# Kernel tuning notes

Measured on AMD Instinct MI355X. Metric: run time of the kernel, lower is better.

## Reference

```python
import jax, jax.numpy as jnp
import numpy as np

INPUT_SIZE, HIDDEN, OUTPUT, NUM_LAYERS = 128, 512, 64, 2
BATCH, SEQ = 64, 256


def setup_inputs() -> dict:
    key = jax.random.key(0)
    ks = jax.random.split(key, 4 * NUM_LAYERS + 3)
    s = 1.0 / np.sqrt(HIDDEN)  # PyTorch LSTM/Linear init scale
    inp = {"x": jax.random.normal(ks[0], (BATCH, SEQ, INPUT_SIZE), dtype=jnp.float32)}
    in_sz = INPUT_SIZE
    for l in range(NUM_LAYERS):
        k0, k1, k2, k3 = ks[1 + 4 * l:5 + 4 * l]
        inp[f"W_ih_{l}"] = jax.random.uniform(k0, (4 * HIDDEN, in_sz), minval=-s, maxval=s, dtype=jnp.float32)
        inp[f"W_hh_{l}"] = jax.random.uniform(k1, (4 * HIDDEN, HIDDEN), minval=-s, maxval=s, dtype=jnp.float32)
        inp[f"b_ih_{l}"] = jax.random.uniform(k2, (4 * HIDDEN,), minval=-s, maxval=s, dtype=jnp.float32)
        inp[f"b_hh_{l}"] = jax.random.uniform(k3, (4 * HIDDEN,), minval=-s, maxval=s, dtype=jnp.float32)
        in_sz = HIDDEN
    inp["W_fc"] = jax.random.uniform(ks[-2], (OUTPUT, HIDDEN), minval=-s, maxval=s, dtype=jnp.float32)
    inp["b_fc"] = jax.random.uniform(ks[-1], (OUTPUT,), minval=-s, maxval=s, dtype=jnp.float32)
    return inp


def _lstm_layer(x, W_ih, W_hh, b_ih, b_hh):
    # x: [B, T, D]. Precompute input-side gates for all timesteps (one big GEMM).
    B = x.shape[0]
    H = W_hh.shape[1]
    xg = jnp.einsum('btd,gd->btg', x, W_ih) + b_ih + b_hh  # [B, T, 4H]
    xg = jnp.swapaxes(xg, 0, 1)  # [T, B, 4H]

    def step(carry, xt):
        h, c = carry
        g = xt + h @ W_hh.T  # [B, 4H]; gate order i, f, g, o (PyTorch)
        i = jax.nn.sigmoid(g[:, 0 * H:1 * H])
        f = jax.nn.sigmoid(g[:, 1 * H:2 * H])
        gg = jnp.tanh(g[:, 2 * H:3 * H])
        o = jax.nn.sigmoid(g[:, 3 * H:4 * H])
        c = f * c + i * gg
        h = o * jnp.tanh(c)
        return (h, c), h

    h0 = jnp.zeros((B, H), dtype=x.dtype)
    (_, _), hs = jax.lax.scan(step, (h0, h0), xg)
    return jnp.swapaxes(hs, 0, 1)  # [B, T, H]


def reference(x, W_ih_0, W_hh_0, b_ih_0, b_hh_0, W_ih_1, W_hh_1, b_ih_1, b_hh_1, W_fc, b_fc):
    h = _lstm_layer(x, W_ih_0, W_hh_0, b_ih_0, b_hh_0)
    h = _lstm_layer(h, W_ih_1, W_hh_1, b_ih_1, b_hh_1)
    last = h[:, -1, :]  # [B, H]
    return last @ W_fc.T + b_fc  # [B, OUTPUT]
```

## Files before the change

### kernel.cpp

```cpp
#include <hip/hip_runtime.h>


#define NB    64
#define SEQL  256
#define INF   128
#define HID   512
#define OUTN  64
#define NWG   256
#define NT    256
#define NCNT  32
#define CADD  (NWG / NCNT)
#define PBOUND 8192

typedef __attribute__((ext_vector_type(8))) short  short8;
typedef __attribute__((ext_vector_type(4))) float  floatx4;
typedef unsigned short u16;
typedef unsigned long long u64;

#define TIE4(N, x0,x1,x2,x3)                                                \
  asm volatile("s_waitcnt vmcnt(" N ")" : "+v"(x0), "+v"(x1), "+v"(x2), "+v"(x3))
#define TIE3(N, x0,x1,x2)                                                   \
  asm volatile("s_waitcnt vmcnt(" N ")" : "+v"(x0), "+v"(x1), "+v"(x2))
#define TIE2(N, x0,x1)                                                      \
  asm volatile("s_waitcnt vmcnt(" N ")" : "+v"(x0), "+v"(x1))

#define MFMA(ACC, A, B) \
  ACC = __builtin_amdgcn_mfma_f32_16x16x32_bf16((A), (B), ACC, 0, 0, 0)

__device__ __forceinline__ u16 f2bf(float f) {
  union { float f; unsigned u; } v; v.f = f;
  return (u16)((v.u + 0x7FFFu + ((v.u >> 16) & 1u)) >> 16);
}
__device__ __forceinline__ float bf2f(u16 s) {
  union { unsigned u; float f; } v; v.u = ((unsigned)s) << 16;
  return v.f;
}
__device__ __forceinline__ float sigf(float v) {
  return __builtin_amdgcn_rcpf(1.f + __expf(-v));
}
__device__ __forceinline__ float tanh_fast(float v) {
  float cv = fminf(fmaxf(v, -15.f), 15.f);
  float e = __expf(2.f * cv);
  return (e - 1.f) * __builtin_amdgcn_rcpf(e + 1.f);
}

__device__ __forceinline__ short8 ldh(const u16* p) {
  short8 d;
  asm volatile("global_load_dwordx4 %0, %1, off sc0 sc1" : "=v"(d) : "v"(p));
  return d;
}
__device__ __forceinline__ void st8c(u16* p, u64 v) {
  __hip_atomic_store((u64*)p, v, __ATOMIC_RELAXED, __HIP_MEMORY_SCOPE_AGENT);
}

__device__ __forceinline__ int swz(int gi) {
  return (gi * 16) ^ (((gi >> 6) & 7) << 4);
}

__device__ __forceinline__ void wait_ge(const unsigned* f0, int thr0,
                                        const unsigned* f1, int thr1) {
  const int lane = threadIdx.x & 63;
  const unsigned* fp = nullptr;
  int thr = 0;
  if (lane < 16)      { fp = f0 + lane;        thr = thr0; }
  else if (lane < 32) { fp = f1 + (lane - 16); thr = thr1; }
  if (thr <= 0) fp = nullptr;
  for (int i = 0; i < PBOUND; ++i) {
    int v = 0x7fffffff;
    if (fp) v = (int)__hip_atomic_load(fp, __ATOMIC_RELAXED,
                                       __HIP_MEMORY_SCOPE_AGENT);
    if (__all(v >= thr)) break;
    if (i > 2048) __builtin_amdgcn_s_sleep(2);
  }
  __builtin_amdgcn_sched_barrier(0);
  asm volatile("" ::: "memory");
}

__device__ __forceinline__ void grid_bar_once(unsigned* leaf, int w) {
  asm volatile("s_waitcnt vmcnt(0)" ::: "memory");
  __syncthreads();
  if (threadIdx.x == 0)
    __hip_atomic_fetch_add(&leaf[(w & (NCNT - 1)) * 32], 1u, __ATOMIC_RELAXED,
                           __HIP_MEMORY_SCOPE_AGENT);
  if (threadIdx.x < 64) {
    const int lane = threadIdx.x & 63;
    for (int i = 0; i < (1 << 16); ++i) {
      unsigned v = CADD;
      if (lane < NCNT)
        v = __hip_atomic_load(&leaf[lane * 32], __ATOMIC_RELAXED,
                              __HIP_MEMORY_SCOPE_AGENT);
      if (__all(v >= CADD)) break;
      __builtin_amdgcn_s_sleep(1);
    }
  }
  __syncthreads();
}

__device__ __forceinline__ floatx4 xpose4(floatx4 v, int jb0, int jb1) {
  floatx4 t;
#pragma unroll
  for (int r = 0; r < 4; ++r) t[r] = __shfl_xor(v[r], 1);
  floatx4 u;
  u[0] = jb0 ? t[1] : v[0];
  u[1] = jb0 ? v[1] : t[0];
  u[2] = jb0 ? t[3] : v[2];
  u[3] = jb0 ? v[3] : t[2];
  floatx4 s;
#pragma unroll
  for (int r = 0; r < 4; ++r) s[r] = __shfl_xor(u[r], 2);
  floatx4 w_;
  w_[0] = jb1 ? s[2] : u[0];
  w_[1] = jb1 ? s[3] : u[1];
  w_[2] = jb1 ? u[2] : s[0];
  w_[3] = jb1 ? u[3] : s[1];
  return w_;
}

template <int KS, int KIN>
__device__ __forceinline__ void load_B(short8 (&Bf)[2][32],
                                       const float* __restrict__ Wih,
                                       const float* __restrict__ Whh,
                                       int li, int wv, int mrow, int quad) {
#pragma unroll
  for (int t2 = 0; t2 < 2; ++t2) {
    const int rowid = wv * 32 + t2 * 16 + mrow;
    const int r = (rowid & 3) * HID + 32 * li + (rowid >> 2);
    const float* wr = Wih + (size_t)r * KIN;
    const float* hr = Whh + (size_t)r * HID - KIN;
#pragma unroll
    for (int ks = 0; ks < KS; ++ks) {
      short8 v;
#pragma unroll
      for (int j = 0; j < 8; ++j) {
        const int k = 32 * ks + quad * 8 + j;
        v[j] = (short)f2bf(k < KIN ? wr[k] : hr[k]);
      }
      Bf[t2][ks] = v;
    }
  }
}

__global__ __launch_bounds__(NT, 1) void lstm_groups(
    const float* __restrict__ x,
    const float* __restrict__ Wih0, const float* __restrict__ Whh0,
    const float* __restrict__ bih0, const float* __restrict__ bhh0,
    const float* __restrict__ Wih1, const float* __restrict__ Whh1,
    const float* __restrict__ bih1, const float* __restrict__ bhh1,
    const float* __restrict__ Wfc,  const float* __restrict__ bfc,
    float* __restrict__ out,
    unsigned* __restrict__ leaf,
    unsigned* __restrict__ flag0, unsigned* __restrict__ flag1,
    u16* __restrict__ h0r, u16* __restrict__ h1r, u16* __restrict__ xg)
{
  const int w = blockIdx.x, tid = threadIdx.x;
  const int lane = tid & 63, wv = tid >> 6;
  const int quad = lane >> 4, mrow = lane & 15;
  const int g = w & 7, m = w >> 3;
  const bool isL1 = (m >= 16);
  const int  li   = isL1 ? m - 16 : m;

  __shared__ u64   h_lds8[8][8];
  __shared__ float red[16][17];
  __shared__ short8 hA2[2][512];
  __shared__ short8 hB[512];
  char* hAc = (char*)hA2;
  char* hBc = (char*)hB;

#pragma unroll
  for (int i = 0; i < 8; ++i) {
    const int s = w * 8 + i, gs = s >> 8, ts = s & 255;
    u16* dst = xg + (size_t)(gs * 256 + ts) * 1024;
    const int b = tid >> 5, k0 = (tid & 31) * 4;
    const float* src = x + ((size_t)(8 * gs + b) * SEQL + ts) * INF + k0;
    union { u16 h[4]; u64 u; } pk;
#pragma unroll
    for (int j = 0; j < 4; ++j) pk.h[j] = f2bf(src[j]);
    st8c(dst + b * 128 + k0, pk.u);
  }

  short8 Bf[2][32];
  if (isL1) load_B<32, HID>(Bf, Wih1, Whh1, li, wv, mrow, quad);
  else      load_B<20, INF>(Bf, Wih0, Whh0, li, wv, mrow, quad);
  float bsA, bsB;
  {
    const int r0 = wv * 32 + mrow, r1 = r0 + 16;
    const int ra = (r0 & 3) * HID + 32 * li + (r0 >> 2);
    const int rb = (r1 & 3) * HID + 32 * li + (r1 >> 2);
    bsA = isL1 ? (bih1[ra] + bhh1[ra]) : (bih0[ra] + bhh0[ra]);
    bsB = isL1 ? (bih1[rb] + bhh1[rb]) : (bih0[rb] + bhh0[rb]);
  }

  grid_bar_once(leaf, w);

  unsigned* flag0g = flag0 + g * 64;
  unsigned* flag1g = flag1 + g * 64;
  u16* h0g = h0r + (size_t)g * 32768;
  u16* h1g = h1r + (size_t)g * 32768;
  const u16* xgg = xg + (size_t)g * 256 * 1024;

  const int q4 = quad;
  const int m4 = mrow >> 2, jg = mrow & 3;
  const int jb0 = jg & 1, jb1 = (jg >> 1) & 1;
  float cstA = 0.f, cstB = 0.f;
  const int ab = mrow & 7;
  const int koff = quad * 8;

  const bool ldr = (wv != 0);
  const int base = tid - 64;

  if (isL1) {
    wait_ge(flag0g, 1, flag1g, 0);
    short8 s0 = ldh(h0g + tid * 8);
    short8 s1 = ldh(h0g + (tid + 256) * 8);
    TIE2("0", s0, s1);
    *(short8*)(hAc + swz(tid)) = s0;
    *(short8*)(hAc + swz(tid + 256)) = s1;
    __syncthreads();
  }

  for (int t = 0; t < SEQL; ++t) {
    floatx4 a00 = {bsA, bsA, bsA, bsA}, a01 = {0,0,0,0};
    floatx4 a10 = {bsB, bsB, bsB, bsB}, a11 = {0,0,0,0};
    const int pb = (t & 1) * 8192;
    const int nb_ = ((t + 1) & 1) * 8192;

    if (!isL1) {
      const u16* xa = xgg + (size_t)t * 1024 + ab * 128 + koff;
      short8 x0 = *(const short8*)(xa +  0);
      short8 x1 = *(const short8*)(xa + 32);
      short8 x2 = *(const short8*)(xa + 64);
      short8 x3 = *(const short8*)(xa + 96);
      MFMA(a00,x0,Bf[0][0]);  MFMA(a10,x0,Bf[1][0]);
      MFMA(a01,x1,Bf[0][1]);  MFMA(a11,x1,Bf[1][1]);
      MFMA(a00,x2,Bf[0][2]);  MFMA(a10,x2,Bf[1][2]);
      MFMA(a01,x3,Bf[0][3]);  MFMA(a11,x3,Bf[1][3]);

      if (ldr) {
        wait_ge(flag0g, t, flag1g, t - 7);
        const u16* src = h0g + ((t + 7) & 7) * 4096;
        const bool g2 = (base < 128);
        short8 s0 = ldh(src + base * 8);
        short8 s1 = ldh(src + (base + 192) * 8);
        short8 s2;
        if (g2) s2 = ldh(src + (base + 384) * 8);
        if (g2) { TIE3("0", s0, s1, s2); }
        else    { TIE2("0", s0, s1); }
        *(short8*)(hAc + swz(base)) = s0;
        *(short8*)(hAc + swz(base + 192)) = s1;
        if (g2) *(short8*)(hAc + swz(base + 384)) = s2;
      }
      __syncthreads();

#pragma unroll
      for (int n = 0; n < 16; ++n) {
        const short8 fv = *(const short8*)(
            hAc + ((ab * 1024 + n * 64 + quad * 16) ^ (ab << 4)));
        if ((n & 1) == 0) { MFMA(a00, fv, Bf[0][4 + n]); MFMA(a10, fv, Bf[1][4 + n]); }
        else              { MFMA(a01, fv, Bf[0][4 + n]); MFMA(a11, fv, Bf[1][4 + n]); }
      }
    } else {
      short8 b0, b1, b2, p0, p1, p2;
      bool g2 = false;
      if (ldr) {
        const int thr0 = (t + 2 < 256) ? (t + 2) : 256;
        wait_ge(flag0g, thr0, flag1g, t);
        const u16* srcB = h1g + ((t + 7) & 7) * 4096;
        const u16* srcP = h0g + ((t + 1) & 7) * 4096;
        g2 = (base < 128);
        b0 = ldh(srcB + base * 8);
        b1 = ldh(srcB + (base + 192) * 8);
        if (g2) b2 = ldh(srcB + (base + 384) * 8);
        p0 = ldh(srcP + base * 8);
        p1 = ldh(srcP + (base + 192) * 8);
        if (g2) p2 = ldh(srcP + (base + 384) * 8);
      }

#pragma unroll
      for (int n = 0; n < 16; ++n) {
        const short8 fv = *(const short8*)(
            hAc + pb + ((ab * 1024 + n * 64 + quad * 16) ^ (ab << 4)));
        if ((n & 1) == 0) { MFMA(a00, fv, Bf[0][n]); MFMA(a10, fv, Bf[1][n]); }
        else              { MFMA(a01, fv, Bf[0][n]); MFMA(a11, fv, Bf[1][n]); }
      }

      if (ldr) {
        if (g2) { TIE3("3", b0, b1, b2); }
        else    { TIE2("2", b0, b1); }
        *(short8*)(hBc + swz(base)) = b0;
        *(short8*)(hBc + swz(base + 192)) = b1;
        if (g2) *(short8*)(hBc + swz(base + 384)) = b2;
        if (g2) { TIE3("0", p0, p1, p2); }
        else    { TIE2("0", p0, p1); }
        *(short8*)(hAc + nb_ + swz(base)) = p0;
        *(short8*)(hAc + nb_ + swz(base + 192)) = p1;
        if (g2) *(short8*)(hAc + nb_ + swz(base + 384)) = p2;
      }
      __syncthreads();

#pragma unroll
      for (int n = 0; n < 16; ++n) {
        const short8 fv = *(const short8*)(
            hBc + ((ab * 1024 + n * 64 + quad * 16) ^ (ab << 4)));
        if ((n & 1) == 0) { MFMA(a00, fv, Bf[0][16 + n]); MFMA(a10, fv, Bf[1][16 + n]); }
        else              { MFMA(a01, fv, Bf[0][16 + n]); MFMA(a11, fv, Bf[1][16 + n]); }
      }
    }

    const floatx4 vA = a00 + a01, vB = a10 + a11;
    if (lane < 32) {
      const floatx4 gA = xpose4(vA, jb0, jb1);
      const floatx4 gB = xpose4(vB, jb0, jb1);
      const float cA = sigf(gA[1]) * cstA + sigf(gA[0]) * tanh_fast(gA[2]);
      const float cB = sigf(gB[1]) * cstB + sigf(gB[0]) * tanh_fast(gB[2]);
      cstA = cA; cstB = cB;
      u16* hl = (u16*)&h_lds8[q4 * 4 + jg][0];
      hl[wv * 8 + m4]     = f2bf(sigf(gA[3]) * tanh_fast(cA));
      hl[wv * 8 + m4 + 4] = f2bf(sigf(gB[3]) * tanh_fast(cB));
    }
    __syncthreads();

    if (tid < 64) {
      const int b = tid >> 3, u8 = tid & 7;
      const u64 v = h_lds8[b][u8];
      u16* dst = (isL1 ? h1g : h0g) + (t & 7) * 4096 + b * 512 + li * 32 + u8 * 4;
      st8c(dst, v);
    }
    asm volatile("s_waitcnt vmcnt(0)" ::: "memory");
    if (tid == 0)
      __hip_atomic_store((isL1 ? flag1g : flag0g) + li, (unsigned)(t + 1),
                         __ATOMIC_RELAXED, __HIP_MEMORY_SCOPE_AGENT);
  }

  wait_ge(flag1g, 256, flag1g, 0);
  {
    const int bloc = m >> 2, oq = m & 3;
    const int ol = tid >> 4, ksub = tid & 15;
    const u16* hp = h1g + 7 * 4096 + bloc * 512 + ksub * 32;
    short8 v0 = ldh(hp),      v1 = ldh(hp + 8);
    short8 v2 = ldh(hp + 16), v3 = ldh(hp + 24);
    TIE4("0", v0, v1, v2, v3);
    const float* wr = Wfc + (size_t)(oq * 16 + ol) * HID + ksub * 32;
    float s = 0.f;
#pragma unroll
    for (int j = 0; j < 8; ++j) {
      s += bf2f((u16)v0[j]) * wr[j];
      s += bf2f((u16)v1[j]) * wr[8 + j];
      s += bf2f((u16)v2[j]) * wr[16 + j];
      s += bf2f((u16)v3[j]) * wr[24 + j];
    }
    red[ol][ksub] = s;
    __syncthreads();
    if (tid < 16) {
      float sum = 0.f;
#pragma unroll
      for (int j = 0; j < 16; ++j) sum += red[tid][j];
      out[(size_t)(8 * g + bloc) * OUTN + oq * 16 + tid] = sum + bfc[oq * 16 + tid];
    }
  }
}


extern "C" void kernel_launch(void* const* d_in, const int* in_sizes, int n_in,
                              void* d_out, int out_size, void* d_ws, size_t ws_size,
                              hipStream_t stream) {
  (void)in_sizes; (void)n_in; (void)out_size; (void)ws_size;

  char* ws = (char*)d_ws;
  unsigned* leaf  = (unsigned*)(ws + 256);
  unsigned* flag0 = (unsigned*)(ws + 8192);
  unsigned* flag1 = (unsigned*)(ws + 16384);
  u16* h0r = (u16*)(ws + 32768);
  u16* h1r = (u16*)(ws + 557056);
  u16* xg  = (u16*)(ws + 1081344);

  hipMemsetAsync(d_ws, 0, 1081344, stream);

  const float* x    = (const float*)d_in[0];
  const float* Wih0 = (const float*)d_in[1];
  const float* Whh0 = (const float*)d_in[2];
  const float* bih0 = (const float*)d_in[3];
  const float* bhh0 = (const float*)d_in[4];
  const float* Wih1 = (const float*)d_in[5];
  const float* Whh1 = (const float*)d_in[6];
  const float* bih1 = (const float*)d_in[7];
  const float* bhh1 = (const float*)d_in[8];
  const float* Wfc  = (const float*)d_in[9];
  const float* bfc  = (const float*)d_in[10];
  float* out = (float*)d_out;

  void* args[] = {
    (void*)&x,
    (void*)&Wih0, (void*)&Whh0, (void*)&bih0, (void*)&bhh0,
    (void*)&Wih1, (void*)&Whh1, (void*)&bih1, (void*)&bhh1,
    (void*)&Wfc,  (void*)&bfc,
    (void*)&out,
    (void*)&leaf, (void*)&flag0, (void*)&flag1,
    (void*)&h0r, (void*)&h1r, (void*)&xg
  };
  hipError_t err = hipLaunchCooperativeKernel((const void*)lstm_groups,
                                              dim3(NWG), dim3(NT), args, 0, stream);
  if (err != hipSuccess) {
    hipLaunchKernelGGL(lstm_groups, dim3(NWG), dim3(NT), 0, stream,
                       x, Wih0, Whh0, bih0, bhh0, Wih1, Whh1, bih1, bhh1,
                       Wfc, bfc, out, leaf, flag0, flag1, h0r, h1r, xg);
  }
}
```

Measured before the change: 948.8 us.

## Replace flag polling with sentinel-valid data polling on 16-slot hidden-state rings

Consumers stop waiting on per-step producer flags and instead poll the hidden-state ring data directly, treating 0xFFFF bf16 values as not-yet-written sentinels, so the flag round-trip is removed from the recurrent critical path. The rings grow from 8 to 16 slots with slot 0 as the zero initial state. Layer-1 work-groups re-poison consumed slots with the sentinel to allow reuse. This adds extra memsets, sentinel-reset traffic and tricky ordering that could race or break if a real hidden value ever encodes as 0xFFFF (a NaN pattern, so unlikely).

```diff
diff --git a/kernel.cpp b/kernel.cpp
--- a/kernel.cpp
+++ b/kernel.cpp
@@ -19,8 +19,6 @@
 
 #define TIE4(N, x0,x1,x2,x3)                                                \
   asm volatile("s_waitcnt vmcnt(" N ")" : "+v"(x0), "+v"(x1), "+v"(x2), "+v"(x3))
-#define TIE3(N, x0,x1,x2)                                                   \
-  asm volatile("s_waitcnt vmcnt(" N ")" : "+v"(x0), "+v"(x1), "+v"(x2))
 #define TIE2(N, x0,x1)                                                      \
   asm volatile("s_waitcnt vmcnt(" N ")" : "+v"(x0), "+v"(x1))
 
@@ -52,23 +50,25 @@
 __device__ __forceinline__ void st8c(u16* p, u64 v) {
   __hip_atomic_store((u64*)p, v, __ATOMIC_RELAXED, __HIP_MEMORY_SCOPE_AGENT);
 }
+__device__ __forceinline__ unsigned ldf(const unsigned* p) {
+  return __hip_atomic_load(p, __ATOMIC_RELAXED, __HIP_MEMORY_SCOPE_AGENT);
+}
+
+__device__ __forceinline__ bool valid8(short8 v) {
+  return ((u16)v[0] != 0xFFFFu) & ((u16)v[4] != 0xFFFFu);
+}
 
 __device__ __forceinline__ int swz(int gi) {
   return (gi * 16) ^ (((gi >> 6) & 7) << 4);
 }
 
-__device__ __forceinline__ void wait_ge(const unsigned* f0, int thr0,
-                                        const unsigned* f1, int thr1) {
+__device__ __forceinline__ void wait_ge(const unsigned* f, int thr) {
+  if (thr <= 0) return;
   const int lane = threadIdx.x & 63;
-  const unsigned* fp = nullptr;
-  int thr = 0;
-  if (lane < 16)      { fp = f0 + lane;        thr = thr0; }
-  else if (lane < 32) { fp = f1 + (lane - 16); thr = thr1; }
-  if (thr <= 0) fp = nullptr;
+  const unsigned* p = (lane < 16) ? f + lane : nullptr;
   for (int i = 0; i < PBOUND; ++i) {
     int v = 0x7fffffff;
-    if (fp) v = (int)__hip_atomic_load(fp, __ATOMIC_RELAXED,
-                                       __HIP_MEMORY_SCOPE_AGENT);
+    if (p) v = (int)ldf(p);
     if (__all(v >= thr)) break;
     if (i > 2048) __builtin_amdgcn_s_sleep(2);
   }
@@ -86,9 +86,7 @@
     const int lane = threadIdx.x & 63;
     for (int i = 0; i < (1 << 16); ++i) {
       unsigned v = CADD;
-      if (lane < NCNT)
-        v = __hip_atomic_load(&leaf[lane * 32], __ATOMIC_RELAXED,
-                              __HIP_MEMORY_SCOPE_AGENT);
+      if (lane < NCNT) v = ldf(&leaf[lane * 32]);
       if (__all(v >= CADD)) break;
       __builtin_amdgcn_s_sleep(1);
     }
@@ -194,8 +192,8 @@
 
   unsigned* flag0g = flag0 + g * 64;
   unsigned* flag1g = flag1 + g * 64;
-  u16* h0g = h0r + (size_t)g * 32768;
-  u16* h1g = h1r + (size_t)g * 32768;
+  u16* h0g = h0r + (size_t)g * 65536;
+  u16* h1g = h1r + (size_t)g * 65536;
   const u16* xgg = xg + (size_t)g * 256 * 1024;
 
   const int q4 = quad;
@@ -207,12 +205,20 @@
 
   const bool ldr = (wv != 0);
   const int base = tid - 64;
+  int c0 = -1, c1 = -1;
 
   if (isL1) {
-    wait_ge(flag0g, 1, flag1g, 0);
-    short8 s0 = ldh(h0g + tid * 8);
-    short8 s1 = ldh(h0g + (tid + 256) * 8);
-    TIE2("0", s0, s1);
+    const u16* sp = h0g + 1 * 4096;
+    short8 s0 = {}, s1 = {};
+    bool done = false;
+    for (int it = 0; it < PBOUND && !done; ++it) {
+      s0 = ldh(sp + tid * 8);
+      s1 = ldh(sp + (tid + 256) * 8);
+      TIE2("0", s0, s1);
+      done = __all(valid8(s0) & valid8(s1));
+      if (it > 2048) __builtin_amdgcn_s_sleep(2);
+    }
+    __builtin_amdgcn_sched_barrier(0);
     *(short8*)(hAc + swz(tid)) = s0;
     *(short8*)(hAc + swz(tid + 256)) = s1;
     __syncthreads();
@@ -223,6 +229,7 @@
     floatx4 a10 = {bsB, bsB, bsB, bsB}, a11 = {0,0,0,0};
     const int pb = (t & 1) * 8192;
     const int nb_ = ((t + 1) & 1) * 8192;
+    const int thr = t - 8;
 
     if (!isL1) {
       const u16* xa = xgg + (size_t)t * 1024 + ab * 128 + koff;
@@ -236,15 +243,22 @@
       MFMA(a01,x3,Bf[0][3]);  MFMA(a11,x3,Bf[1][3]);
 
       if (ldr) {
-        wait_ge(flag0g, t, flag1g, t - 7);
-        const u16* src = h0g + ((t + 7) & 7) * 4096;
+        const u16* src = h0g + (t & 15) * 4096;
         const bool g2 = (base < 128);
-        short8 s0 = ldh(src + base * 8);
-        short8 s1 = ldh(src + (base + 192) * 8);
-        short8 s2;
-        if (g2) s2 = ldh(src + (base + 384) * 8);
-        if (g2) { TIE3("0", s0, s1, s2); }
-        else    { TIE2("0", s0, s1); }
+        short8 s0 = {}, s1 = {}, s2 = {};
+        bool done = false;
+        for (int it = 0; it < PBOUND && !done; ++it) {
+          s0 = ldh(src + base * 8);
+          s1 = ldh(src + (base + 192) * 8);
+          if (g2) s2 = ldh(src + (base + 384) * 8);
+          int fl = 0x7fffffff;
+          if (lane < 16 && thr > 0) fl = (int)ldf(flag1g + lane);
+          asm volatile("s_waitcnt vmcnt(0)" : "+v"(s0), "+v"(s1), "+v"(s2));
+          bool v = valid8(s0) & valid8(s1) & (!g2 | valid8(s2)) & (fl >= thr);
+          done = __all(v);
+          if (it > 2048) __builtin_amdgcn_s_sleep(2);
+        }
+        __builtin_amdgcn_sched_barrier(0);
         *(short8*)(hAc + swz(base)) = s0;
         *(short8*)(hAc + swz(base + 192)) = s1;
         if (g2) *(short8*)(hAc + swz(base + 384)) = s2;
@@ -259,41 +273,67 @@
         else              { MFMA(a01, fv, Bf[0][4 + n]); MFMA(a11, fv, Bf[1][4 + n]); }
       }
     } else {
-      short8 b0, b1, b2, p0, p1, p2;
-      bool g2 = false;
+      const bool pf = (t < 255);
       if (ldr) {
-        const int thr0 = (t + 2 < 256) ? (t + 2) : 256;
-        wait_ge(flag0g, thr0, flag1g, t);
-        const u16* srcB = h1g + ((t + 7) & 7) * 4096;
-        const u16* srcP = h0g + ((t + 1) & 7) * 4096;
-        g2 = (base < 128);
+        const u16* srcB = h1g + (t & 15) * 4096;
+        const u16* srcP = h0g + ((t + 2) & 15) * 4096;
+        const bool g2 = (base < 128);
+        short8 b0 = {}, b1 = {}, b2 = {}, p0 = {}, p1 = {}, p2 = {};
         b0 = ldh(srcB + base * 8);
         b1 = ldh(srcB + (base + 192) * 8);
         if (g2) b2 = ldh(srcB + (base + 384) * 8);
-        p0 = ldh(srcP + base * 8);
-        p1 = ldh(srcP + (base + 192) * 8);
-        if (g2) p2 = ldh(srcP + (base + 384) * 8);
-      }
-
-#pragma unroll
-      for (int n = 0; n < 16; ++n) {
-        const short8 fv = *(const short8*)(
-            hAc + pb + ((ab * 1024 + n * 64 + quad * 16) ^ (ab << 4)));
-        if ((n & 1) == 0) { MFMA(a00, fv, Bf[0][n]); MFMA(a10, fv, Bf[1][n]); }
-        else              { MFMA(a01, fv, Bf[0][n]); MFMA(a11, fv, Bf[1][n]); }
-      }
-
-      if (ldr) {
-        if (g2) { TIE3("3", b0, b1, b2); }
-        else    { TIE2("2", b0, b1); }
+        if (pf) {
+          p0 = ldh(srcP + base * 8);
+          p1 = ldh(srcP + (base + 192) * 8);
+          if (g2) p2 = ldh(srcP + (base + 384) * 8);
+        }
+        __builtin_amdgcn_sched_barrier(0);
+#pragma unroll
+        for (int n = 0; n < 16; ++n) {
+          const short8 fv = *(const short8*)(
+              hAc + pb + ((ab * 1024 + n * 64 + quad * 16) ^ (ab << 4)));
+          if ((n & 1) == 0) { MFMA(a00, fv, Bf[0][n]); MFMA(a10, fv, Bf[1][n]); }
+          else              { MFMA(a01, fv, Bf[0][n]); MFMA(a11, fv, Bf[1][n]); }
+        }
+        bool done = false;
+        for (int it = 0; it < PBOUND && !done; ++it) {
+          if (it) {
+            b0 = ldh(srcB + base * 8);
+            b1 = ldh(srcB + (base + 192) * 8);
+            if (g2) b2 = ldh(srcB + (base + 384) * 8);
+            if (pf) {
+              p0 = ldh(srcP + base * 8);
+              p1 = ldh(srcP + (base + 192) * 8);
+              if (g2) p2 = ldh(srcP + (base + 384) * 8);
+            }
+          }
+          int fl = 0x7fffffff;
+          if (lane < 16 && thr > 0) fl = (int)ldf(flag1g + lane);
+          asm volatile("s_waitcnt vmcnt(0)"
+                       : "+v"(b0), "+v"(b1), "+v"(b2),
+                         "+v"(p0), "+v"(p1), "+v"(p2));
+          bool v = valid8(b0) & valid8(b1) & (!g2 | valid8(b2)) & (fl >= thr);
+          if (pf) v = v & valid8(p0) & valid8(p1) & (!g2 | valid8(p2));
+          done = __all(v);
+          if (it > 2048) __builtin_amdgcn_s_sleep(2);
+        }
+        __builtin_amdgcn_sched_barrier(0);
         *(short8*)(hBc + swz(base)) = b0;
         *(short8*)(hBc + swz(base + 192)) = b1;
         if (g2) *(short8*)(hBc + swz(base + 384)) = b2;
-        if (g2) { TIE3("0", p0, p1, p2); }
-        else    { TIE2("0", p0, p1); }
-        *(short8*)(hAc + nb_ + swz(base)) = p0;
-        *(short8*)(hAc + nb_ + swz(base + 192)) = p1;
-        if (g2) *(short8*)(hAc + nb_ + swz(base + 384)) = p2;
+        if (pf) {
+          *(short8*)(hAc + nb_ + swz(base)) = p0;
+          *(short8*)(hAc + nb_ + swz(base + 192)) = p1;
+          if (g2) *(short8*)(hAc + nb_ + swz(base + 384)) = p2;
+        }
+      } else {
+#pragma unroll
+        for (int n = 0; n < 16; ++n) {
+          const short8 fv = *(const short8*)(
+              hAc + pb + ((ab * 1024 + n * 64 + quad * 16) ^ (ab << 4)));
+          if ((n & 1) == 0) { MFMA(a00, fv, Bf[0][n]); MFMA(a10, fv, Bf[1][n]); }
+          else              { MFMA(a01, fv, Bf[0][n]); MFMA(a11, fv, Bf[1][n]); }
+        }
       }
       __syncthreads();
 
@@ -319,23 +359,64 @@
     }
     __syncthreads();
 
-    if (tid < 64) {
-      const int b = tid >> 3, u8 = tid & 7;
-      const u64 v = h_lds8[b][u8];
-      u16* dst = (isL1 ? h1g : h0g) + (t & 7) * 4096 + b * 512 + li * 32 + u8 * 4;
-      st8c(dst, v);
-    }
-    asm volatile("s_waitcnt vmcnt(0)" ::: "memory");
-    if (tid == 0)
-      __hip_atomic_store((isL1 ? flag1g : flag0g) + li, (unsigned)(t + 1),
-                         __ATOMIC_RELAXED, __HIP_MEMORY_SCOPE_AGENT);
-  }
-
-  wait_ge(flag1g, 256, flag1g, 0);
+    if (wv == 0) {
+      u16* ring = isL1 ? h1g : h0g;
+      if (!isL1) {
+        wait_ge(flag1g, t - 7);
+      }
+      {
+        const int b = tid >> 3, u8 = tid & 7;
+        const u64 v = h_lds8[b][u8];
+        st8c(ring + ((t + 1) & 15) * 4096 + b * 512 + li * 32 + u8 * 4, v);
+      }
+      if (isL1) {
+        unsigned vmin = 0x7fffffffu;
+        if (lane < 16)       vmin = ldf(flag0g + lane);
+        else if (lane < 32)  vmin = ldf(flag1g + lane - 16);
+#pragma unroll
+        for (int o = 1; o < 16; o <<= 1) {
+          unsigned ov = (unsigned)__shfl_xor((int)vmin, o);
+          vmin = vmin < ov ? vmin : ov;
+        }
+        const int m0 = __shfl((int)vmin, 0);
+        const int m1 = __shfl((int)vmin, 16);
+        int tgt0 = m0 - 2; if (m1 - 1 < tgt0) tgt0 = m1 - 1;
+        if (t - 1 < tgt0) tgt0 = t - 1;
+        while (c0 <= tgt0) {
+          st8c(h0g + ((c0 + 1) & 15) * 4096 + li * 256 + lane * 4,
+               0xFFFFFFFFFFFFFFFFull);
+          ++c0;
+        }
+        int tgt1 = m1 - 2; if (t - 1 < tgt1) tgt1 = t - 1;
+        while (c1 <= tgt1) {
+          st8c(h1g + ((c1 + 1) & 15) * 4096 + li * 256 + lane * 4,
+               0xFFFFFFFFFFFFFFFFull);
+          ++c1;
+        }
+      }
+      asm volatile("s_waitcnt vmcnt(0)" ::: "memory");
+      if (tid == 0)
+        __hip_atomic_store((isL1 ? flag1g : flag0g) + li, (unsigned)(t + 1),
+                           __ATOMIC_RELAXED, __HIP_MEMORY_SCOPE_AGENT);
+    }
+  }
+
+  {
+    const int lane_ = tid & 63;
+    const unsigned* p = (lane_ < 16) ? flag1g + lane_ : nullptr;
+    for (int i = 0; i < PBOUND; ++i) {
+      int v = 0x7fffffff;
+      if (p) v = (int)ldf(p);
+      if (__all(v >= 256)) break;
+      if (i > 2048) __builtin_amdgcn_s_sleep(2);
+    }
+    __builtin_amdgcn_sched_barrier(0);
+    asm volatile("" ::: "memory");
+  }
   {
     const int bloc = m >> 2, oq = m & 3;
     const int ol = tid >> 4, ksub = tid & 15;
-    const u16* hp = h1g + 7 * 4096 + bloc * 512 + ksub * 32;
+    const u16* hp = h1g + 0 * 4096 + bloc * 512 + ksub * 32;
     short8 v0 = ldh(hp),      v1 = ldh(hp + 8);
     short8 v2 = ldh(hp + 16), v3 = ldh(hp + 24);
     TIE4("0", v0, v1, v2, v3);
@@ -370,10 +451,15 @@
   unsigned* flag0 = (unsigned*)(ws + 8192);
   unsigned* flag1 = (unsigned*)(ws + 16384);
   u16* h0r = (u16*)(ws + 32768);
-  u16* h1r = (u16*)(ws + 557056);
-  u16* xg  = (u16*)(ws + 1081344);
-
-  hipMemsetAsync(d_ws, 0, 1081344, stream);
+  u16* h1r = (u16*)(ws + 1081344);
+  u16* xg  = (u16*)(ws + 2129920);
+
+  hipMemsetAsync(d_ws, 0, 32768, stream);
+  hipMemsetAsync(ws + 32768, 0xFF, 2097152, stream);
+  for (int gg = 0; gg < 8; ++gg) {
+    hipMemsetAsync(ws + 32768   + gg * 131072, 0, 8192, stream);
+    hipMemsetAsync(ws + 1081344 + gg * 131072, 0, 8192, stream);
+  }
 
   const float* x    = (const float*)d_in[0];
   const float* Wih0 = (const float*)d_in[1];
```

After: 1.266 ms. +33.4%, slower.
